# Kernel tuning notes

Hardware: AMD Instinct MI355X
Metric: run time of the kernel (lower is better)

## Reference

```python
import jax, jax.numpy as jnp
import numpy as np

L = 8192   # sequence length
B = 4      # batch
D = 512    # embed_dim
NDIM = 16  # EMA state dim
Z = 128    # shared q/k dim
W = 128    # attention window
MP = 256   # max relative positions
NEG = -50000.0  # TOKEN_SELF_ATTN_VALUE-style mask fill


def setup_inputs() -> dict:
    key = jax.random.key(0)
    ks = jax.random.split(key, 16)
    def tn(k, shp, std):  # truncated-normal-ish init (clipped normal)
        return jnp.clip(jax.random.normal(k, shp) * std, -2 * std, 2 * std)
    val = jnp.ones((NDIM, 1)).at[1::2].set(-1.0)  # MultiHeadEMA beta init pattern
    return {
        "x": jax.random.normal(ks[0], (L, B, D), dtype=jnp.float32),
        "delta": tn(ks[1], (D, NDIM, 1), 0.2),
        "alpha": tn(ks[2], (D, NDIM, 1), 0.2),
        "beta": tn(ks[3], (D, NDIM, 1), 0.02) + val,
        "gamma": jax.random.normal(ks[4], (D, NDIM)),
        "omega": jax.random.normal(ks[5], (D,)),
        "Wp": tn(ks[6], (D, 1), 0.02),      # LatentConfigurator weight_proj
        "bp": jnp.zeros((1,)),
        "temp": jnp.array([0.5 * np.log(D)], dtype=jnp.float32),  # log(sqrt(D))
        "Wz": tn(ks[7], (D, Z), 0.02),
        "qg": jax.random.normal(ks[8], (Z,)) * 0.02 + 1.0,
        "qb": jnp.zeros((Z,)),
        "kg": jax.random.normal(ks[9], (Z,)) * 0.02 + 1.0,
        "kb": jnp.zeros((Z,)),
        "Wv": tn(ks[10], (D, D), 0.02),
        "relb": tn(ks[11], (2 * MP - 1,), 0.02),  # FastRelativePositionalBias table
    }


def _rotary(t, cos, sin):
    # t: (B, L, Z); cos/sin: (L, Z//2). Complex rotation on interleaved pairs.
    t1, t2 = t[..., 0::2], t[..., 1::2]
    return jnp.stack([t1 * cos - t2 * sin, t1 * sin + t2 * cos], axis=-1).reshape(t.shape)


def _forward(x, delta, alpha, beta, gamma, omega, Wp, bp, temp, Wz, qg, qb, kg, kb, Wv, relb):
    scale = 1.0 / np.sqrt(NDIM)
    # ---- MultiHeadEMA: damped EMA as long convolution via FFT ----
    p = jax.nn.sigmoid(delta)                      # (D,N,1)
    a = jax.nn.sigmoid(alpha)
    logq = jnp.log1p(-(p * a))                     # log(1 - p*alpha)
    t = jnp.arange(L, dtype=jnp.float32)
    kern = (p * beta) * jnp.exp(logq * t)          # (D,N,L) Vandermonde kernel
    k1d = jnp.einsum('dnl,dn->dl', kern, gamma * scale)  # (D,L)
    xb = x.transpose(1, 2, 0)                      # (B,D,L)
    conv = jnp.fft.irfft(jnp.fft.rfft(xb, n=2 * L) * jnp.fft.rfft(k1d, n=2 * L), n=2 * L)[..., :L]
    mx = jax.nn.silu(conv.transpose(2, 0, 1) + x * omega)  # (L,B,D)
    # ---- LatentConfigurator: sigmoid token routing (proj_dim==1) ----
    pi = jax.nn.sigmoid((mx @ Wp + bp) / jnp.exp(temp))[..., 0].T  # (B,L)
    mxb = mx.transpose(1, 0, 2)                    # (B,L,D)
    sel = pi > 0.5
    idx = jnp.cumsum(sel.astype(jnp.int32), axis=1) * sel  # (B,L); 0 -> dropped slot
    counts = sel.sum(axis=1)                       # (B,)
    bi = jnp.arange(B)[:, None]
    # compress_seq: scatter selected tokens to compact prefix (slot 0 dropped)
    c = jnp.zeros((B, L + 1, D), mx.dtype).at[bi, idx].add(mxb * sel[..., None])[:, 1:]
    # ---- windowed attention over compressed tokens ----
    z = jax.nn.silu(c @ Wz)                        # (B,L,Z)
    freqs = 1.0 / (10000.0 ** (jnp.arange(0, Z, 2, dtype=jnp.float32) / Z))
    ang = jnp.arange(L, dtype=jnp.float32)[:, None] * freqs
    cos, sin = jnp.cos(ang), jnp.sin(ang)
    q = _rotary(z * qg + qb, cos, sin)
    kk = _rotary(z * kg + kb, cos, sin)
    v = jax.nn.silu(c @ Wv)                        # (B,L,D)
    n = L // W
    qw = q.reshape(B, n, W, Z)
    def look_around(tw):  # prepend previous window: (B,n,W,f) -> (B,n,2W,f)
        prev = jnp.pad(tw, ((0, 0), (1, 0), (0, 0), (0, 0)))[:, :-1]
        return jnp.concatenate([prev, tw], axis=2)
    kw = look_around(kk.reshape(B, n, W, Z))
    vw = look_around(v.reshape(B, n, W, D))
    base = (jnp.arange(n) * W)[:, None, None]
    qabs = base + jnp.arange(W)[None, :, None]         # (n,W,1)
    kabs = base + jnp.arange(-W, W)[None, None, :]     # (n,1,2W)
    mask = (kabs <= qabs) & (kabs >= 0) & (kabs[None] < counts[:, None, None, None])  # (B,n,W,2W)
    rel = jnp.arange(-W, W)[None, :] - jnp.arange(W)[:, None]   # (W,2W)
    bias = relb[jnp.clip(rel + MP - 1, 0, 2 * MP - 2)]          # (W,2W)
    scores = jnp.einsum('bnwz,bnkz->bnwk', qw, kw) / np.sqrt(Z) + bias
    attn = jax.nn.softmax(jnp.where(mask, scores, NEG), axis=-1)
    h = jnp.einsum('bnwk,bnkd->bnwd', attn, vw).reshape(B, L, D)
    # ---- extract: gather back to original positions, gate by pi ----
    hpad = jnp.concatenate([jnp.zeros((B, 1, D), h.dtype), h], axis=1)
    hsel = jnp.take_along_axis(hpad, idx[..., None], axis=1)    # (B,L,D)
    return x + (hsel * pi[..., None]).transpose(1, 0, 2)        # (L,B,D)


def reference(x, delta, alpha, beta, gamma, omega, Wp, bp, temp, Wz, qg, qb, kg, kb, Wv, relb):
    return _forward(x, delta, alpha, beta, gamma, omega, Wp, bp, temp, Wz, qg, qb, kg, kb, Wv, relb)
```

## Files before the change

kernel.cpp:

```cpp
#include <hip/hip_runtime.h>
#include <math.h>

constexpr int L = 8192;
constexpr int B = 4;
constexpr int D = 512;
constexpr int NDIM = 16;
constexpr int Z = 128;
constexpr float NEGF = -50000.0f;
constexpr int CCL = 32;
constexpr int NCH = L / CCL;
constexpr int FMAX = 64;

typedef short s16x8 __attribute__((ext_vector_type(8)));
typedef float f32x4 __attribute__((ext_vector_type(4)));

typedef __attribute__((address_space(1))) const void* as1cv;
typedef __attribute__((address_space(3))) void* as3v;

__device__ __forceinline__ void gld16(const void* g, void* l) {
  __builtin_amdgcn_global_load_lds((as1cv)g, (as3v)l, 16, 0, 0);
}

__device__ __forceinline__ unsigned short f2bf(float f) {
  unsigned u = __builtin_bit_cast(unsigned, f);
  u += 0x7fffu + ((u >> 16) & 1u);
  return (unsigned short)(u >> 16);
}

#define DPPADD(acc, ctrl, rmask)                                                   \
  {                                                                                \
    int _mv = __builtin_amdgcn_update_dpp(0, __builtin_bit_cast(int, acc),         \
                                          ctrl, rmask, 0xf, false);                \
    acc += __builtin_bit_cast(float, _mv);                                         \
  }

__global__ __launch_bounds__(256) void k_prep(const float* __restrict__ delta,
                                              const float* __restrict__ alpha,
                                              const float* __restrict__ beta,
                                              const float* __restrict__ gamma,
                                              double* __restrict__ qdn,
                                              double* __restrict__ cdn,
                                              double* __restrict__ rp1,
                                              double* __restrict__ rp2,
                                              float* __restrict__ qf,
                                              float* __restrict__ cf,
                                              float* __restrict__ r1f,
                                              float* __restrict__ r2f,
                                              float* __restrict__ r3f,
                                              int* __restrict__ fcnt) {
  int i = blockIdx.x * 256 + threadIdx.x;
  if (i == 0) *fcnt = 0;
  if (i >= D * NDIM) return;
  double p = 1.0 / (1.0 + exp(-(double)delta[i]));
  double a = 1.0 / (1.0 + exp(-(double)alpha[i]));
  double q = 1.0 - p * a;
  double c = p * (double)beta[i] * (double)gamma[i] * 0.25;
  qdn[i] = q; cdn[i] = c;
  double q2 = q * q, q4 = q2 * q2, q8 = q4 * q4;
  double q16 = q8 * q8, q32 = q16 * q16, q64 = q32 * q32;
  rp1[i] = q64;
  rp2[i] = q64 * q64;
  qf[i] = (float)q; cf[i] = (float)c;
  r1f[i] = (float)q32;
  r2f[i] = (float)q64;
  r3f[i] = (float)(q64 * q32);
}

__global__ __launch_bounds__(256) void k_tab(float2* __restrict__ tab) {
  int tid = blockIdx.x * 256 + threadIdx.x;
  int i = tid & 63, j = tid >> 6;
  double freq = exp(((double)(-2 * i) / 128.0) * log(10000.0));
  float angf = (float)j * (float)freq;
  double sa, ca;
  sincos((double)angf, &sa, &ca);
  float2 r; r.x = (float)ca; r.y = (float)sa;
  tab[tid] = r;
}

__global__ __launch_bounds__(256, 4) void k_convA(const float* __restrict__ x,
                                                  const float* __restrict__ qf,
                                                  float* __restrict__ E) {
  int bx = blockIdx.x;
  int tile = bx & 63, dg = (bx >> 6) & 7, b = bx >> 9;
  int dl = threadIdx.x & 63, cl = threadIdx.x >> 6;
  int dgl = dg * 64 + dl;
  int t = tile * 4 + cl;
  float q[NDIM], s[NDIM];
#pragma unroll
  for (int n = 0; n < NDIM; ++n) { q[n] = qf[dgl * NDIM + n]; s[n] = 0.f; }
  const float* xp = x + ((size_t)(t * CCL) * B + b) * D + dgl;
  float xv[CCL];
#pragma unroll
  for (int u = 0; u < CCL; ++u) xv[u] = xp[u * (B * D)];
#pragma unroll
  for (int u = 0; u < CCL; ++u) {
#pragma unroll
    for (int n = 0; n < NDIM; ++n) s[n] = fmaf(q[n], s[n], xv[u]);
  }
  float* eb = E + ((size_t)(b * NCH + t) * NDIM) * 512 + dgl;
#pragma unroll
  for (int n = 0; n < NDIM; ++n) eb[(size_t)n * 512] = s[n];
}

__global__ __launch_bounds__(256, 4) void k_convC(const float* __restrict__ x,
                                                  const float* __restrict__ omega,
                                                  const float* __restrict__ qf,
                                                  const float* __restrict__ cf,
                                                  const float* __restrict__ r1f,
                                                  const float* __restrict__ r2f,
                                                  const float* __restrict__ r3f,
                                                  const float* __restrict__ E,
                                                  const float* __restrict__ Wp,
                                                  unsigned short* __restrict__ mxb,
                                                  float* __restrict__ pdot) {
  int bx = blockIdx.x;
  int tile = bx & 63, dg = (bx >> 6) & 7, b = bx >> 9;
  int dl = threadIdx.x & 63, cl = threadIdx.x >> 6;
  int dgl = dg * 64 + dl;
  int t = tile * 4 + cl;
  float q[NDIM], c[NDIM], s[NDIM];
#pragma unroll
  for (int n = 0; n < NDIM; ++n) {
    q[n] = qf[dgl * NDIM + n];
    c[n] = cf[dgl * NDIM + n];
    s[n] = 0.f;
  }
  if (t >= 1) {
    const float* e1 = E + ((size_t)(b * NCH + t - 1) * NDIM) * 512 + dgl;
#pragma unroll
    for (int n = 0; n < NDIM; ++n) s[n] = e1[(size_t)n * 512];
  }
  if (t >= 2) {
    const float* e2 = E + ((size_t)(b * NCH + t - 2) * NDIM) * 512 + dgl;
#pragma unroll
    for (int n = 0; n < NDIM; ++n) s[n] = fmaf(r1f[dgl * NDIM + n], e2[(size_t)n * 512], s[n]);
  }
  if (t >= 3) {
    const float* e3 = E + ((size_t)(b * NCH + t - 3) * NDIM) * 512 + dgl;
#pragma unroll
    for (int n = 0; n < NDIM; ++n) s[n] = fmaf(r2f[dgl * NDIM + n], e3[(size_t)n * 512], s[n]);
  }
  if (t >= 4) {
    const float* e4 = E + ((size_t)(b * NCH + t - 4) * NDIM) * 512 + dgl;
#pragma unroll
    for (int n = 0; n < NDIM; ++n) s[n] = fmaf(r3f[dgl * NDIM + n], e4[(size_t)n * 512], s[n]);
  }
  float om = omega[dgl];
  float wp = Wp[dgl];
  const float* xp = x + ((size_t)(t * CCL) * B + b) * D + dgl;
  unsigned short* mp = mxb + ((size_t)b * L + t * CCL) * 512 + dgl;
  float* pp = pdot + ((size_t)(b * L + t * CCL)) * 8 + dg;
  float xv[CCL];
#pragma unroll
  for (int u = 0; u < CCL; ++u) xv[u] = xp[u * (B * D)];
#pragma unroll
  for (int u = 0; u < CCL; ++u) {
#pragma unroll
    for (int n = 0; n < NDIM; ++n) s[n] = fmaf(q[n], s[n], xv[u]);
    float p0 = c[0] * s[0], p1 = c[1] * s[1], p2 = c[2] * s[2], p3 = c[3] * s[3];
    p0 = fmaf(c[4], s[4], p0);  p1 = fmaf(c[5], s[5], p1);
    p2 = fmaf(c[6], s[6], p2);  p3 = fmaf(c[7], s[7], p3);
    p0 = fmaf(c[8], s[8], p0);  p1 = fmaf(c[9], s[9], p1);
    p2 = fmaf(c[10], s[10], p2); p3 = fmaf(c[11], s[11], p3);
    p0 = fmaf(c[12], s[12], p0); p1 = fmaf(c[13], s[13], p1);
    p2 = fmaf(c[14], s[14], p2); p3 = fmaf(c[15], s[15], p3);
    float conv = (p0 + p1) + (p2 + p3);
    float m = fmaf(xv[u], om, conv);
    float v = m / (1.0f + __expf(-m));
    mp[(size_t)u * 512] = f2bf(v);
    float pd = v * wp;
    DPPADD(pd, 0x111, 0xf);
    DPPADD(pd, 0x112, 0xf);
    DPPADD(pd, 0x114, 0xf);
    DPPADD(pd, 0x118, 0xf);
    DPPADD(pd, 0x142, 0xa);
    DPPADD(pd, 0x143, 0x8);
    if (dl == 63) pp[(size_t)u * 8] = pd;
  }
}

__global__ __launch_bounds__(256) void k_logitc(const float* __restrict__ pdot,
                                                const float* __restrict__ bp,
                                                const float* __restrict__ temp,
                                                float* __restrict__ pi,
                                                int* __restrict__ selb,
                                                int* __restrict__ fcnt,
                                                int* __restrict__ flags) {
  int rid = blockIdx.x * 256 + threadIdx.x;
  const float* pr = pdot + (size_t)rid * 8;
  double acc = 0.0;
#pragma unroll
  for (int j = 0; j < 8; ++j) acc += (double)pr[j];
  double logit = acc + (double)bp[0];
  pi[rid] = (float)(1.0 / (1.0 + exp(-logit / exp((double)temp[0]))));
  selb[rid] = (logit > 0.0) ? 1 : 0;
  if (fabs(logit) < 1e-4) {
    int slot = atomicAdd(fcnt, 1);
    if (slot < FMAX) flags[slot] = rid;
  }
}

__global__ __launch_bounds__(256) void k_fix(const int* __restrict__ fcnt,
                                             const int* __restrict__ flags,
                                             const float* __restrict__ x,
                                             const double* __restrict__ qdn,
                                             const double* __restrict__ cdn,
                                             const double* __restrict__ rp1,
                                             const double* __restrict__ rp2,
                                             const float* __restrict__ omega,
                                             const float* __restrict__ Wp,
                                             double* __restrict__ pfix) {
  int nb = blockIdx.x;
  int fi = nb >> 3, dblk = nb & 7;
  int count = *fcnt; if (count > FMAX) count = FMAX;
  if (fi >= count) return;
  int rid = flags[fi];
  int b = rid >> 13, l = rid & (L - 1);
  int t = l >> 6, io = l & 63;
  int sub = threadIdx.x >> 6, dl = threadIdx.x & 63;
  int d = dblk * 64 + dl;
  double q[NDIM], s[NDIM];
#pragma unroll
  for (int n = 0; n < NDIM; ++n) { q[n] = qdn[d * NDIM + n]; s[n] = 0.0; }
  int c0 = (sub < 3) ? (t - 3 + sub) : t;
  int steps = (sub < 3) ? 64 : (io + 1);
  if (c0 >= 0) {
    const float* xp = x + ((size_t)(c0 * 64) * B + b) * D + d;
    for (int i = 0; i < steps; ++i) {
      double xv = (double)xp[(size_t)i * (B * D)];
#pragma unroll
      for (int n = 0; n < NDIM; ++n) s[n] = fma(q[n], s[n], xv);
    }
  }
  __shared__ double Esm[4][64][NDIM];
#pragma unroll
  for (int n = 0; n < NDIM; ++n) Esm[sub][dl][n] = s[n];
  __syncthreads();
  if (sub == 3) {
    double sfin[NDIM];
#pragma unroll
    for (int n = 0; n < NDIM; ++n) {
      double base = q[n], r = 1.0;
      int e = io + 1;
      while (e) { if (e & 1) r *= base; base *= base; e >>= 1; }
      double S = Esm[2][dl][n] + rp1[d * NDIM + n] * Esm[1][dl][n] + rp2[d * NDIM + n] * Esm[0][dl][n];
      sfin[n] = Esm[3][dl][n] + r * S;
    }
    double conv = 0.0;
#pragma unroll
    for (int n = 0; n < NDIM; ++n) conv = fma(cdn[d * NDIM + n], sfin[n], conv);
    double xv = (double)x[((size_t)l * B + b) * D + d];
    double m = conv + xv * (double)omega[d];
    double mxd = m / (1.0 + exp(-m));
    double v = mxd * (double)Wp[d];
#pragma unroll
    for (int off = 32; off; off >>= 1) v += __shfl_down(v, off, 64);
    if (dl == 0) pfix[fi * 8 + dblk] = v;
  }
}

__global__ __launch_bounds__(64) void k_fix2(const int* __restrict__ fcnt,
                                             const int* __restrict__ flags,
                                             const double* __restrict__ pfix,
                                             const float* __restrict__ bp,
                                             const float* __restrict__ temp,
                                             float* __restrict__ pi,
                                             int* __restrict__ selb) {
  int fi = threadIdx.x;
  int count = *fcnt; if (count > FMAX) count = FMAX;
  if (fi >= count) return;
  double s = 0.0;
#pragma unroll
  for (int j = 0; j < 8; ++j) s += pfix[fi * 8 + j];
  double logit = s + (double)bp[0];
  int rid = flags[fi];
  selb[rid] = (logit > 0.0) ? 1 : 0;
  pi[rid] = (float)(1.0 / (1.0 + exp(-logit / exp((double)temp[0]))));
}

__global__ __launch_bounds__(256) void k_scan(const int* __restrict__ selb,
                                              int* __restrict__ idx,
                                              int* __restrict__ src,
                                              int* __restrict__ counts) {
  int b = blockIdx.x;
  int t = threadIdx.x;
  __shared__ int part[256];
  const int PER = L / 256;
  int base = b * L + t * PER;
  int loc[PER];
  int cnt = 0;
#pragma unroll
  for (int i = 0; i < PER; ++i) { loc[i] = selb[base + i]; cnt += loc[i]; }
  part[t] = cnt;
  __syncthreads();
  for (int off = 1; off < 256; off <<= 1) {
    int v = (t >= off) ? part[t - off] : 0;
    __syncthreads();
    part[t] += v;
    __syncthreads();
  }
  int run = (t == 0) ? 0 : part[t - 1];
#pragma unroll
  for (int i = 0; i < PER; ++i) {
    int sflag = loc[i];
    run += sflag;
    idx[base + i] = sflag ? run : 0;
    if (sflag) src[b * L + run - 1] = t * PER + i;
  }
  if (t == 255) counts[b] = part[255];
  __syncthreads();
  int total = part[255];
  for (int i2 = total + t; i2 < L; i2 += 256) src[b * L + i2] = 0;
}

__global__ __launch_bounds__(256) void k_wt(const float* __restrict__ Wm,
                                            unsigned short* __restrict__ Wt, int N) {
  int idx = blockIdx.x * 256 + threadIdx.x;
  int n = idx >> 9, kk = idx & 511;
  Wt[idx] = f2bf(Wm[(size_t)kk * N + n]);
}

__global__ __launch_bounds__(256) void k_gemm_mfma(const unsigned short* __restrict__ mxb,
                                                   const int* __restrict__ src,
                                                   const int* __restrict__ counts,
                                                   const unsigned short* __restrict__ Bt,
                                                   float* __restrict__ outF,
                                                   unsigned short* __restrict__ outT,
                                                   int N, int mode) {
  __shared__ char smem[32768];
  char* As = smem;
  char* Bs = smem + 16384;
  int tid = threadIdx.x;
  int w = tid >> 6, l = tid & 63;
  int mtile, ntile;
  if (mode == 1) {
    int lin = blockIdx.y * 256 + blockIdx.x;
    int xcd = lin & 7, loc = lin >> 3;
    mtile = xcd * 32 + (loc >> 2);
    ntile = loc & 3;
  } else {
    mtile = blockIdx.x; ntile = blockIdx.y;
  }
  int m0 = mtile * 128, n0 = ntile * 128;
  int gb = m0 >> 13, j0 = m0 & 8191;
  if (j0 >= counts[gb]) return;
  int wr = w >> 1, wc = w & 1;
  const unsigned short* arow[4];
  const unsigned short* brow[4];
#pragma unroll
  for (int ld = 0; ld < 4; ++ld) {
    int li = w * 4 + ld;
    int row = li * 8 + (l >> 3);
    int col = ((l & 7) ^ (row & 7)) << 3;
    int srow = src[gb * 8192 + j0 + row];
    arow[ld] = mxb + ((size_t)gb * 8192 + srow) * 512 + col;
    brow[ld] = Bt + (size_t)(n0 + row) * 512 + col;
  }
  f32x4 acc[4][4];
  f32x4 zz = {0.f, 0.f, 0.f, 0.f};
#pragma unroll
  for (int mi = 0; mi < 4; ++mi)
#pragma unroll
    for (int ni = 0; ni < 4; ++ni) acc[mi][ni] = zz;

  for (int k0 = 0; k0 < 512; k0 += 64) {
#pragma unroll
    for (int ld = 0; ld < 4; ++ld) {
      int li = w * 4 + ld;
      gld16(arow[ld] + k0, As + li * 1024);
      gld16(brow[ld] + k0, Bs + li * 1024);
    }
    __syncthreads();
    s16x8 af[4][2], bfr[4][2];
#pragma unroll
    for (int kh = 0; kh < 2; ++kh) {
#pragma unroll
      for (int mi = 0; mi < 4; ++mi) {
        int row = wr * 64 + mi * 16 + (l & 15);
        int byte = row * 128 + ((kh * 64 + ((l >> 4) * 16)) ^ ((row & 7) << 4));
        af[mi][kh] = *(const s16x8*)(As + byte);
      }
#pragma unroll
      for (int ni = 0; ni < 4; ++ni) {
        int row = wc * 64 + ni * 16 + (l & 15);
        int byte = row * 128 + ((kh * 64 + ((l >> 4) * 16)) ^ ((row & 7) << 4));
        bfr[ni][kh] = *(const s16x8*)(Bs + byte);
      }
    }
#pragma unroll
    for (int kh = 0; kh < 2; ++kh)
#pragma unroll
      for (int mi = 0; mi < 4; ++mi)
#pragma unroll
        for (int ni = 0; ni < 4; ++ni)
          acc[mi][ni] = __builtin_amdgcn_mfma_f32_16x16x32_bf16(af[mi][kh], bfr[ni][kh], acc[mi][ni], 0, 0, 0);
    __syncthreads();
  }
  if (mode == 0) {
#pragma unroll
    for (int mi = 0; mi < 4; ++mi)
#pragma unroll
      for (int ni = 0; ni < 4; ++ni)
#pragma unroll
        for (int r = 0; r < 4; ++r) {
          float vv = acc[mi][ni][r];
          vv = vv / (1.0f + __expf(-vv));
          int mrow = m0 + wr * 64 + mi * 16 + (l >> 4) * 4 + r;
          int ncol = n0 + wc * 64 + ni * 16 + (l & 15);
          outF[(size_t)mrow * N + ncol] = vv;
        }
  } else {
#pragma unroll
    for (int mi = 0; mi < 4; ++mi)
#pragma unroll
      for (int ni = 0; ni < 4; ++ni)
#pragma unroll
        for (int r = 0; r < 4; ++r) {
          float vv = acc[mi][ni][r];
          vv = vv / (1.0f + __expf(-vv));
          int mrow = wr * 64 + mi * 16 + (l >> 4) * 4 + r;
          int ncol = wc * 64 + ni * 16 + (l & 15);
          int byteoff = ncol * 256 + ((mrow * 2) ^ ((ncol & 7) << 4));
          *(unsigned short*)(smem + byteoff) = f2bf(vv);
        }
    __syncthreads();
#pragma unroll
    for (int it = 0; it < 8; ++it) {
      int ncol = w * 32 + it * 4 + (l >> 4);
      int ch = l & 15;
      int byteoff = ncol * 256 + ((ch * 16) ^ ((ncol & 7) << 4));
      s16x8 vch = *(const s16x8*)(smem + byteoff);
      *(s16x8*)(outT + ((size_t)(gb * 512 + n0 + ncol)) * 8192 + j0 + ch * 8) = vch;
    }
  }
}

__global__ __launch_bounds__(256) void k_rot(const float* __restrict__ z,
                                             const float2* __restrict__ tab,
                                             const int* __restrict__ counts,
                                             const float* __restrict__ qg,
                                             const float* __restrict__ qb,
                                             const float* __restrict__ kg,
                                             const float* __restrict__ kb,
                                             unsigned short* __restrict__ qo,
                                             unsigned short* __restrict__ ko) {
  int tid = blockIdx.x * 256 + threadIdx.x;
  int i = tid & 63;
  int row = tid >> 6;
  int j = row & (L - 1);
  int b = row >> 13;
  if (j >= counts[b]) return;
  float2 cs = tab[j * 64 + i];
  float cc = cs.x, ss = cs.y;
  size_t base = (size_t)row * Z + 2 * i;
  float z1 = z[base], z2 = z[base + 1];
  float q1 = z1 * qg[2 * i] + qb[2 * i], q2 = z2 * qg[2 * i + 1] + qb[2 * i + 1];
  float k1 = z1 * kg[2 * i] + kb[2 * i], k2 = z2 * kg[2 * i + 1] + kb[2 * i + 1];
  qo[base]     = f2bf(q1 * cc - q2 * ss);
  qo[base + 1] = f2bf(q1 * ss + q2 * cc);
  ko[base]     = f2bf(k1 * cc - k2 * ss);
  ko[base + 1] = f2bf(k1 * ss + k2 * cc);
}

__global__ __launch_bounds__(256) void k_attn_mfma(const unsigned short* __restrict__ q,
                                                   const unsigned short* __restrict__ k,
                                                   const unsigned short* __restrict__ vT,
                                                   const float* __restrict__ relb,
                                                   const int* __restrict__ counts,
                                                   const int* __restrict__ src,
                                                   const float* __restrict__ pi,
                                                   const float* __restrict__ x,
                                                   float* __restrict__ out) {
  __shared__ char smem[81920];
  char* Qs = smem;
  char* Ks = smem + 16384;
  char* Ps = smem;
  char* Vs = smem + 32768;
  int tid = threadIdx.x, w = tid >> 6, l = tid & 63;
  int bid = blockIdx.x;
  int n = bid >> 3, b = (bid >> 1) & 3, half = bid & 1;
  int cnt = counts[b];
  int q0 = n * 128 + half * 64;
  if (q0 >= cnt) return;
  int kbase = n * 128 - 128;
  const size_t rowb = (size_t)b * L;

#pragma unroll
  for (int ld = 0; ld < 4; ++ld) {
    int li = w * 4 + ld;
    int row = li * 4 + (l >> 4);
    int colb = ((l & 15) * 16) ^ ((row & 7) << 4);
    gld16((const char*)(q + (rowb + q0 + row) * Z) + colb, Qs + li * 1024);
  }
#pragma unroll
  for (int ld = 0; ld < 16; ++ld) {
    int li = w * 16 + ld;
    int row = li * 4 + (l >> 4);
    int jk = kbase + row; if (jk < 0) jk = 0;
    int colb = ((l & 15) * 16) ^ ((row & 7) << 4);
    gld16((const char*)(k + (rowb + jk) * Z) + colb, Ks + li * 1024);
  }
  __syncthreads();

  int m0 = w * 16;
  f32x4 s[16];
  f32x4 zz = {0.f, 0.f, 0.f, 0.f};
#pragma unroll
  for (int ni = 0; ni < 16; ++ni) s[ni] = zz;
  s16x8 aq[4];
#pragma unroll
  for (int ks = 0; ks < 4; ++ks) {
    int row = m0 + (l & 15);
    int byte = row * 256 + ((ks * 64 + ((l >> 4) * 16)) ^ ((row & 7) << 4));
    aq[ks] = *(const s16x8*)(Qs + byte);
  }
#pragma unroll
  for (int ni = 0; ni < 16; ++ni) {
    int row = ni * 16 + (l & 15);
    int rb = row * 256, sw = (row & 7) << 4;
#pragma unroll
    for (int ks = 0; ks < 4; ++ks) {
      s16x8 bk = *(const s16x8*)(Ks + rb + ((ks * 64 + ((l >> 4) * 16)) ^ sw));
      s[ni] = __builtin_amdgcn_mfma_f32_16x16x32_bf16(aq[ks], bk, s[ni], 0, 0, 0);
    }
  }
  __syncthreads();

  auto stageV = [&](int nc) {
#pragma unroll
    for (int ld = 0; ld < 8; ++ld) {
      int li = w * 8 + ld;
      int row = li * 2 + (l >> 5);
      int colb = ((l & 31) * 16) ^ ((row & 7) << 4);
      int j = kbase + (colb >> 1);
      if (j < 0) j = 0;
      gld16((const char*)(vT + ((size_t)(b * 512 + nc * 64 + row)) * L + j), Vs + li * 1024);
    }
  };
  stageV(0);

  int rgrp = (l >> 4) * 4;
  float mxr[4] = {-3e38f, -3e38f, -3e38f, -3e38f};
#pragma unroll
  for (int ni = 0; ni < 16; ++ni) {
    int col = ni * 16 + (l & 15);
    int kabs = kbase + col;
#pragma unroll
    for (int r = 0; r < 4; ++r) {
      int ww = half * 64 + m0 + rgrp + r;
      bool valid = (kabs >= 0) && (kabs <= n * 128 + ww) && (kabs < cnt);
      float vv = valid ? (s[ni][r] * 0.08838834764831845f + relb[col + 127 - ww]) : NEGF;
      s[ni][r] = vv;
      mxr[r] = fmaxf(mxr[r], vv);
    }
  }
#pragma unroll
  for (int r = 0; r < 4; ++r)
    for (int off = 1; off < 16; off <<= 1)
      mxr[r] = fmaxf(mxr[r], __shfl_xor(mxr[r], off, 64));
  float smr[4] = {0.f, 0.f, 0.f, 0.f};
#pragma unroll
  for (int ni = 0; ni < 16; ++ni)
#pragma unroll
    for (int r = 0; r < 4; ++r) {
      float p = __expf(s[ni][r] - mxr[r]);
      s[ni][r] = p;
      smr[r] += p;
    }
#pragma unroll
  for (int r = 0; r < 4; ++r) {
    for (int off = 1; off < 16; off <<= 1) smr[r] += __shfl_xor(smr[r], off, 64);
    smr[r] = 1.0f / smr[r];
  }
#pragma unroll
  for (int ni = 0; ni < 16; ++ni) {
    int colb2 = (ni * 16 + (l & 15)) * 2;
#pragma unroll
    for (int r = 0; r < 4; ++r) {
      int row = m0 + rgrp + r;
      *(unsigned short*)(Ps + row * 512 + (colb2 ^ ((row & 7) << 4))) = f2bf(s[ni][r] * smr[r]);
    }
  }
  __syncthreads();

  s16x8 pa[8];
  {
    int prow = m0 + (l & 15);
    int psw = (prow & 7) << 4;
#pragma unroll
    for (int kt = 0; kt < 8; ++kt)
      pa[kt] = *(const s16x8*)(Ps + prow * 512 + ((kt * 64 + ((l >> 4) * 16)) ^ psw));
  }

  int tlr[4]; float pvr[4]; bool vr[4];
#pragma unroll
  for (int r = 0; r < 4; ++r) {
    int jq = q0 + m0 + rgrp + r;
    vr[r] = (jq < cnt);
    int tl = vr[r] ? src[(b << 13) + jq] : 0;
    tlr[r] = tl;
    pvr[r] = pi[(b << 13) + tl];
  }

  for (int nc = 0; nc < 8; ++nc) {
    if (nc) {
      __syncthreads();
      stageV(nc);
      __syncthreads();
    }
    f32x4 o[4];
#pragma unroll
    for (int ni = 0; ni < 4; ++ni) o[ni] = zz;
#pragma unroll
    for (int kt = 0; kt < 4; ++kt) {
      s16x8 pa0 = pa[kt * 2];
      s16x8 pa1 = pa[kt * 2 + 1];
#pragma unroll
      for (int ni = 0; ni < 4; ++ni) {
        int vrow = ni * 16 + (l & 15);
        int vsw = (vrow & 7) << 4;
        s16x8 vb0 = *(const s16x8*)(Vs + vrow * 512 + ((kt * 128 + ((l >> 4) * 16)) ^ vsw));
        s16x8 vb1 = *(const s16x8*)(Vs + vrow * 512 + ((kt * 128 + 64 + ((l >> 4) * 16)) ^ vsw));
        o[ni] = __builtin_amdgcn_mfma_f32_16x16x32_bf16(pa0, vb0, o[ni], 0, 0, 0);
        o[ni] = __builtin_amdgcn_mfma_f32_16x16x32_bf16(pa1, vb1, o[ni], 0, 0, 0);
      }
    }
#pragma unroll
    for (int ni = 0; ni < 4; ++ni)
#pragma unroll
      for (int r = 0; r < 4; ++r)
        if (vr[r]) {
          size_t off = ((size_t)tlr[r] * B + b) * 512 + nc * 64 + ni * 16 + (l & 15);
          out[off] = fmaf(o[ni][r], pvr[r], x[off]);
        }
  }
}

__global__ __launch_bounds__(256) void k_fill(const float* __restrict__ x,
                                              const int* __restrict__ idx,
                                              float* __restrict__ out) {
  int e4 = blockIdx.x * 256 + threadIdx.x;
  int rem = e4 >> 7;
  int b = rem & 3;
  int l = rem >> 2;
  if (idx[(b << 13) + l] == 0)
    ((float4*)out)[e4] = ((const float4*)x)[e4];
}

extern "C" void kernel_launch(void* const* d_in, const int* in_sizes, int n_in,
                              void* d_out, int out_size, void* d_ws, size_t ws_size,
                              hipStream_t stream) {
  const float* x     = (const float*)d_in[0];
  const float* delta = (const float*)d_in[1];
  const float* alpha = (const float*)d_in[2];
  const float* beta  = (const float*)d_in[3];
  const float* gamma = (const float*)d_in[4];
  const float* omega = (const float*)d_in[5];
  const float* Wp    = (const float*)d_in[6];
  const float* bp    = (const float*)d_in[7];
  const float* temp  = (const float*)d_in[8];
  const float* Wz    = (const float*)d_in[9];
  const float* qg    = (const float*)d_in[10];
  const float* qb    = (const float*)d_in[11];
  const float* kg    = (const float*)d_in[12];
  const float* kb    = (const float*)d_in[13];
  const float* Wv    = (const float*)d_in[14];
  const float* relb  = (const float*)d_in[15];
  (void)in_sizes; (void)n_in; (void)out_size; (void)ws_size;

  char* wsb = (char*)d_ws;
  size_t o = 0;
  auto alloc = [&](size_t bytes) {
    char* p = wsb + o;
    o += (bytes + 255) & ~(size_t)255;
    return p;
  };
  unsigned short* mxb  = (unsigned short*)alloc((size_t)B * L * D * 2);
  float* Ebuf          = (float*)alloc((size_t)B * NCH * NDIM * 512 * 4);
  float* zb            = (float*)alloc((size_t)B * L * Z * 4);
  unsigned short* qb2  = (unsigned short*)alloc((size_t)B * L * Z * 2);
  unsigned short* kb2  = (unsigned short*)alloc((size_t)B * L * Z * 2);
  unsigned short* vTb  = (unsigned short*)alloc((size_t)B * D * L * 2);
  unsigned short* wzt  = (unsigned short*)alloc((size_t)Z * 512 * 2);
  unsigned short* wvt  = (unsigned short*)alloc((size_t)D * 512 * 2);
  float2* tab = (float2*)alloc((size_t)L * 64 * 8);
  float* pdot = (float*)alloc((size_t)B * L * 8 * 4);
  float* pib  = (float*)alloc((size_t)B * L * 4);
  int* selb   = (int*)alloc((size_t)B * L * 4);
  int* idx    = (int*)alloc((size_t)B * L * 4);
  int* src    = (int*)alloc((size_t)B * L * 4);
  int* cnt    = (int*)alloc(256);
  double* qdn = (double*)alloc((size_t)D * NDIM * 8);
  double* cdn = (double*)alloc((size_t)D * NDIM * 8);
  double* rp1 = (double*)alloc((size_t)D * NDIM * 8);
  double* rp2 = (double*)alloc((size_t)D * NDIM * 8);
  float* qf   = (float*)alloc((size_t)D * NDIM * 4);
  float* cf   = (float*)alloc((size_t)D * NDIM * 4);
  float* r1f  = (float*)alloc((size_t)D * NDIM * 4);
  float* r2f  = (float*)alloc((size_t)D * NDIM * 4);
  float* r3f  = (float*)alloc((size_t)D * NDIM * 4);
  int* fcnt   = (int*)alloc(256);
  int* flags  = (int*)alloc(FMAX * 4);
  double* pfix = (double*)alloc((size_t)FMAX * 8 * 8);

  k_prep<<<(D * NDIM + 255) / 256, 256, 0, stream>>>(delta, alpha, beta, gamma,
                                                     qdn, cdn, rp1, rp2, qf, cf, r1f, r2f, r3f, fcnt);
  k_tab<<<L * 64 / 256, 256, 0, stream>>>(tab);
  k_convA<<<B * 8 * 64, 256, 0, stream>>>(x, qf, Ebuf);
  k_convC<<<B * 8 * 64, 256, 0, stream>>>(x, omega, qf, cf, r1f, r2f, r3f, Ebuf, Wp, mxb, pdot);
  k_logitc<<<B * L / 256, 256, 0, stream>>>(pdot, bp, temp, pib, selb, fcnt, flags);
  k_fix<<<FMAX * 8, 256, 0, stream>>>(fcnt, flags, x, qdn, cdn, rp1, rp2, omega, Wp, pfix);
  k_fix2<<<1, 64, 0, stream>>>(fcnt, flags, pfix, bp, temp, pib, selb);
  k_scan<<<B, 256, 0, stream>>>(selb, idx, src, cnt);
  k_wt<<<Z * 512 / 256, 256, 0, stream>>>(Wz, wzt, Z);
  k_wt<<<D * 512 / 256, 256, 0, stream>>>(Wv, wvt, D);
  k_gemm_mfma<<<dim3(256, 1), 256, 0, stream>>>(mxb, src, cnt, wzt, zb, vTb, Z, 0);
  k_gemm_mfma<<<dim3(256, 4), 256, 0, stream>>>(mxb, src, cnt, wvt, zb, vTb, D, 1);
  k_rot<<<B * L * (Z / 2) / 256, 256, 0, stream>>>(zb, tab, cnt, qg, qb, kg, kb, qb2, kb2);
  k_fill<<<(int)((size_t)L * B * D / 4 / 256), 256, 0, stream>>>(x, idx, (float*)d_out);
  k_attn_mfma<<<512, 256, 0, stream>>>(qb2, kb2, vTb, relb, cnt, src, pib, x, (float*)d_out);
}
```

Baseline: 232.3 us.

## Shrink attention LDS footprint and switch rotary table to fast float intrinsics

The attention kernel's shared memory drops from 80KB to 48KB. Q fragments are now loaded straight from global memory into registers, K is staged in two 128-row halves that reuse one buffer, and V is staged in 32-column chunks over 16 iterations instead of 64-column chunks over 8. The goal is to fit more workgroups per CU so latency is better hidden, at the cost of more barriers and more, smaller staging steps. The rotary table kernel also replaces double-precision exp/sincos with fast float intrinsics, which may slightly change the table values for large angles.

```diff
diff --git a/kernel.cpp b/kernel.cpp
--- a/kernel.cpp
+++ b/kernel.cpp
@@ -69,11 +69,11 @@
 __global__ __launch_bounds__(256) void k_tab(float2* __restrict__ tab) {
   int tid = blockIdx.x * 256 + threadIdx.x;
   int i = tid & 63, j = tid >> 6;
-  double freq = exp(((double)(-2 * i) / 128.0) * log(10000.0));
-  float angf = (float)j * (float)freq;
-  double sa, ca;
-  sincos((double)angf, &sa, &ca);
-  float2 r; r.x = (float)ca; r.y = (float)sa;
+  float freq = __expf(((float)(-2 * i) / 128.0f) * 9.210340371976184f);
+  float angf = (float)j * freq;
+  float sa, ca;
+  __sincosf(angf, &sa, &ca);
+  float2 r; r.x = ca; r.y = sa;
   tab[tid] = r;
 }
 
@@ -471,11 +471,9 @@
                                                    const float* __restrict__ pi,
                                                    const float* __restrict__ x,
                                                    float* __restrict__ out) {
-  __shared__ char smem[81920];
-  char* Qs = smem;
-  char* Ks = smem + 16384;
-  char* Ps = smem;
-  char* Vs = smem + 32768;
+  __shared__ char smem[49152];
+  char* A  = smem;
+  char* Bv = smem + 32768;
   int tid = threadIdx.x, w = tid >> 6, l = tid & 63;
   int bid = blockIdx.x;
   int n = bid >> 3, b = (bid >> 1) & 3, half = bid & 1;
@@ -484,62 +482,60 @@
   if (q0 >= cnt) return;
   int kbase = n * 128 - 128;
   const size_t rowb = (size_t)b * L;
-
-#pragma unroll
-  for (int ld = 0; ld < 4; ++ld) {
-    int li = w * 4 + ld;
-    int row = li * 4 + (l >> 4);
-    int colb = ((l & 15) * 16) ^ ((row & 7) << 4);
-    gld16((const char*)(q + (rowb + q0 + row) * Z) + colb, Qs + li * 1024);
-  }
-#pragma unroll
-  for (int ld = 0; ld < 16; ++ld) {
-    int li = w * 16 + ld;
-    int row = li * 4 + (l >> 4);
-    int jk = kbase + row; if (jk < 0) jk = 0;
-    int colb = ((l & 15) * 16) ^ ((row & 7) << 4);
-    gld16((const char*)(k + (rowb + jk) * Z) + colb, Ks + li * 1024);
-  }
-  __syncthreads();
-
   int m0 = w * 16;
+  int lg = l >> 4;
+
+  s16x8 aq[4];
+  {
+    const unsigned short* qrow = q + (rowb + q0 + m0 + (l & 15)) * Z + lg * 8;
+#pragma unroll
+    for (int ks = 0; ks < 4; ++ks) aq[ks] = *(const s16x8*)(qrow + ks * 32);
+  }
+
   f32x4 s[16];
   f32x4 zz = {0.f, 0.f, 0.f, 0.f};
 #pragma unroll
   for (int ni = 0; ni < 16; ++ni) s[ni] = zz;
-  s16x8 aq[4];
-#pragma unroll
-  for (int ks = 0; ks < 4; ++ks) {
-    int row = m0 + (l & 15);
-    int byte = row * 256 + ((ks * 64 + ((l >> 4) * 16)) ^ ((row & 7) << 4));
-    aq[ks] = *(const s16x8*)(Qs + byte);
-  }
-#pragma unroll
-  for (int ni = 0; ni < 16; ++ni) {
-    int row = ni * 16 + (l & 15);
-    int rb = row * 256, sw = (row & 7) << 4;
-#pragma unroll
-    for (int ks = 0; ks < 4; ++ks) {
-      s16x8 bk = *(const s16x8*)(Ks + rb + ((ks * 64 + ((l >> 4) * 16)) ^ sw));
-      s[ni] = __builtin_amdgcn_mfma_f32_16x16x32_bf16(aq[ks], bk, s[ni], 0, 0, 0);
-    }
-  }
-  __syncthreads();
-
-  auto stageV = [&](int nc) {
+#pragma unroll
+  for (int kh2 = 0; kh2 < 2; ++kh2) {
 #pragma unroll
     for (int ld = 0; ld < 8; ++ld) {
       int li = w * 8 + ld;
+      int rowl = li * 4 + (l >> 4);
+      int jk = kbase + kh2 * 128 + rowl;
+      if (jk < 0) jk = 0;
+      int colb = ((l & 15) * 16) ^ ((rowl & 7) << 4);
+      gld16((const char*)(k + (rowb + jk) * Z) + colb, A + li * 1024);
+    }
+    __syncthreads();
+#pragma unroll
+    for (int ni8 = 0; ni8 < 8; ++ni8) {
+      int ni = kh2 * 8 + ni8;
+      int rowl = ni8 * 16 + (l & 15);
+      int rb = rowl * 256, sw = (rowl & 7) << 4;
+#pragma unroll
+      for (int ks = 0; ks < 4; ++ks) {
+        s16x8 bk = *(const s16x8*)(A + rb + ((ks * 64 + lg * 16) ^ sw));
+        s[ni] = __builtin_amdgcn_mfma_f32_16x16x32_bf16(aq[ks], bk, s[ni], 0, 0, 0);
+      }
+    }
+    __syncthreads();
+  }
+
+  auto stageV = [&](int nc) {
+#pragma unroll
+    for (int ld = 0; ld < 4; ++ld) {
+      int li = w * 4 + ld;
       int row = li * 2 + (l >> 5);
       int colb = ((l & 31) * 16) ^ ((row & 7) << 4);
       int j = kbase + (colb >> 1);
       if (j < 0) j = 0;
-      gld16((const char*)(vT + ((size_t)(b * 512 + nc * 64 + row)) * L + j), Vs + li * 1024);
+      gld16((const char*)(vT + ((size_t)(b * 512 + nc * 32 + row)) * L + j), Bv + li * 1024);
     }
   };
   stageV(0);
 
-  int rgrp = (l >> 4) * 4;
+  int rgrp = lg * 4;
   float mxr[4] = {-3e38f, -3e38f, -3e38f, -3e38f};
 #pragma unroll
   for (int ni = 0; ni < 16; ++ni) {
@@ -578,7 +574,7 @@
 #pragma unroll
     for (int r = 0; r < 4; ++r) {
       int row = m0 + rgrp + r;
-      *(unsigned short*)(Ps + row * 512 + (colb2 ^ ((row & 7) << 4))) = f2bf(s[ni][r] * smr[r]);
+      *(unsigned short*)(A + row * 512 + (colb2 ^ ((row & 7) << 4))) = f2bf(s[ni][r] * smr[r]);
     }
   }
   __syncthreads();
@@ -589,7 +585,7 @@
     int psw = (prow & 7) << 4;
 #pragma unroll
     for (int kt = 0; kt < 8; ++kt)
-      pa[kt] = *(const s16x8*)(Ps + prow * 512 + ((kt * 64 + ((l >> 4) * 16)) ^ psw));
+      pa[kt] = *(const s16x8*)(A + prow * 512 + ((kt * 64 + lg * 16) ^ psw));
   }
 
   int tlr[4]; float pvr[4]; bool vr[4];
@@ -602,35 +598,35 @@
     pvr[r] = pi[(b << 13) + tl];
   }
 
-  for (int nc = 0; nc < 8; ++nc) {
+  for (int nc = 0; nc < 16; ++nc) {
     if (nc) {
       __syncthreads();
       stageV(nc);
       __syncthreads();
     }
-    f32x4 o[4];
-#pragma unroll
-    for (int ni = 0; ni < 4; ++ni) o[ni] = zz;
+    f32x4 o[2];
+#pragma unroll
+    for (int ni = 0; ni < 2; ++ni) o[ni] = zz;
 #pragma unroll
     for (int kt = 0; kt < 4; ++kt) {
       s16x8 pa0 = pa[kt * 2];
       s16x8 pa1 = pa[kt * 2 + 1];
 #pragma unroll
-      for (int ni = 0; ni < 4; ++ni) {
+      for (int ni = 0; ni < 2; ++ni) {
         int vrow = ni * 16 + (l & 15);
         int vsw = (vrow & 7) << 4;
-        s16x8 vb0 = *(const s16x8*)(Vs + vrow * 512 + ((kt * 128 + ((l >> 4) * 16)) ^ vsw));
-        s16x8 vb1 = *(const s16x8*)(Vs + vrow * 512 + ((kt * 128 + 64 + ((l >> 4) * 16)) ^ vsw));
+        s16x8 vb0 = *(const s16x8*)(Bv + vrow * 512 + ((kt * 128 + lg * 16) ^ vsw));
+        s16x8 vb1 = *(const s16x8*)(Bv + vrow * 512 + ((kt * 128 + 64 + lg * 16) ^ vsw));
         o[ni] = __builtin_amdgcn_mfma_f32_16x16x32_bf16(pa0, vb0, o[ni], 0, 0, 0);
         o[ni] = __builtin_amdgcn_mfma_f32_16x16x32_bf16(pa1, vb1, o[ni], 0, 0, 0);
       }
     }
 #pragma unroll
-    for (int ni = 0; ni < 4; ++ni)
+    for (int ni = 0; ni < 2; ++ni)
 #pragma unroll
       for (int r = 0; r < 4; ++r)
         if (vr[r]) {
-          size_t off = ((size_t)tlr[r] * B + b) * 512 + nc * 64 + ni * 16 + (l & 15);
+          size_t off = ((size_t)tlr[r] * B + b) * 512 + nc * 32 + ni * 16 + (l & 15);
           out[off] = fmaf(o[ni][r], pvr[r], x[off]);
         }
   }
```

Measured after the change: 230.0 us. No clear change (-1.0%).
